# Kernel tuning notes

Measured on AMD Instinct MI355X. Metric: run time of the kernel, lower is better.

The kernel has to match this reference:

```python
import jax, jax.numpy as jnp
import numpy as np
import math

B, Q, K, D = 16, 2048, 2048, 128


def setup_inputs() -> dict:
    key = jax.random.key(0)
    k1, k2, k3, k4 = jax.random.split(key, 4)
    return {
        "queries": jax.random.normal(k1, (B, Q, D), dtype=jnp.float32),
        "keys": jax.random.normal(k2, (B, K, D), dtype=jnp.float32),
        "values": jax.random.normal(k3, (B, K, D), dtype=jnp.float32),
        "valid_lens": jax.random.randint(k4, (B,), 1, K + 1, dtype=jnp.int32),
    }


def reference(queries, keys, values, valid_lens):
    d = queries.shape[2]
    # scores: [B, Q, K]
    scores = jnp.einsum("bqd,bkd->bqk", queries, keys) / math.sqrt(d)
    # mask: arange(K) < valid_lens[b], broadcast over query dim -> [B, 1, K]
    mask = jnp.arange(scores.shape[-1])[None, None, :] < valid_lens[:, None, None]
    scores = jnp.where(mask, scores, jnp.float32(-1000000.0))
    weights = jax.nn.softmax(scores, axis=-1)
    return jnp.einsum("bqk,bkd->bqd", weights, values)
```

## Files before the change

### kernel.cpp

```cpp
#include <hip/hip_runtime.h>

typedef unsigned short u16;
typedef __bf16 bf16x8 __attribute__((ext_vector_type(8)));
typedef float f32x4 __attribute__((ext_vector_type(4)));

union B8 { uint4 u; bf16x8 v; };
union U8 { u16 s[8]; uint4 u; };

#define NQ 2048
#define NK 2048
#define ND 128

template<int C>
__device__ __forceinline__ float dppf(float x) {
  int v = __builtin_bit_cast(int, x);
  int r = __builtin_amdgcn_update_dpp(v, v, C, 0xF, 0xF, true);
  return __builtin_bit_cast(float, r);
}
__device__ __forceinline__ float rowmax16(float x) {
  x = fmaxf(x, dppf<0xB1>(x));
  x = fmaxf(x, dppf<0x4E>(x));
  x = fmaxf(x, dppf<0x141>(x));
  x = fmaxf(x, dppf<0x140>(x));
  return x;
}
__device__ __forceinline__ float rowsum16(float x) {
  x += dppf<0xB1>(x);
  x += dppf<0x4E>(x);
  x += dppf<0x141>(x);
  x += dppf<0x140>(x);
  return x;
}

__device__ __forceinline__ bf16x8 cvt8(float4 a, float4 b) {
  bf16x8 r;
  r[0] = (__bf16)a.x; r[1] = (__bf16)a.y; r[2] = (__bf16)a.z; r[3] = (__bf16)a.w;
  r[4] = (__bf16)b.x; r[5] = (__bf16)b.y; r[6] = (__bf16)b.z; r[7] = (__bf16)b.w;
  return r;
}

__device__ __forceinline__ void async16(const u16* g, u16* l) {
  __builtin_amdgcn_global_load_lds(
      (const __attribute__((address_space(1))) unsigned int*)g,
      (__attribute__((address_space(3))) unsigned int*)l, 16, 0, 0);
}

__global__ __launch_bounds__(256)
void prepack(const float* __restrict__ kg, const float* __restrict__ vg,
             u16* __restrict__ wk, u16* __restrict__ wvp)
{
  __shared__ __align__(16) u16 sVp[8192];
  const int bt  = blockIdx.x;
  const int tid = threadIdx.x;
  const int srow = tid >> 2, scq = tid & 3;
  const size_t rowoff = (size_t)((bt >> 5) * NK + (bt & 31) * 64 + srow) * ND + scq * 32;

  u16* kimg = wk + (size_t)bt * 8192;
  {
    const float* src = kg + rowoff;
    #pragma unroll
    for (int c = 0; c < 4; ++c) {
      B8 tt; tt.v = cvt8(*(const float4*)(src + c * 8), *(const float4*)(src + c * 8 + 4));
      *(uint4*)(&kimg[srow * 128 + (((scq * 4 + c) ^ (srow & 15)) << 3)]) = tt.u;
    }
  }
  {
    const float* src = vg + rowoff;
    #pragma unroll
    for (int c = 0; c < 4; ++c) {
      B8 x; x.v = cvt8(*(const float4*)(src + c * 8), *(const float4*)(src + c * 8 + 4));
      U8 tt; tt.u = x.u;
      #pragma unroll
      for (int j = 0; j < 8; ++j) {
        int d = scq * 32 + c * 8 + j;
        sVp[d * 64 + (((srow >> 3) ^ j) << 3) + (srow & 7)] = tt.s[j];
      }
    }
  }
  __syncthreads();
  u16* vimg = wvp + (size_t)bt * 8192;
  const uint4* s4 = (const uint4*)sVp;
  uint4* d4 = (uint4*)vimg;
  #pragma unroll
  for (int k = 0; k < 4; ++k) d4[tid + 256 * k] = s4[tid + 256 * k];
}

__global__ __launch_bounds__(1024)
void flash_fwd(const float* __restrict__ qg, const int* __restrict__ vlg,
               float* __restrict__ og,
               const u16* __restrict__ wk, const u16* __restrict__ wvp)
{
  __shared__ __align__(16) u16 smem[81920];
  u16* const sKb = smem;
  u16* const sVb = smem + 32768;
  u16* const sPb = smem + 65536;
  float* const fb = (float*)smem;

  const int tid  = threadIdx.x;
  const int lane = tid & 63;
  const int wv   = tid >> 6;
  const int qw   = wv & 7;
  const int grp  = wv >> 3;
  const int n    = lane & 15;
  const int quad = lane >> 4;

  const int bi = blockIdx.x;
  const int b  = ((bi & 7) << 1) | ((bi >> 3) & 1);
  const int qt = bi >> 4;

  const int vl = vlg[b];
  const int nt = (vl + 63) >> 6;

  const int qrow0 = qt * 128 + qw * 16;

  bf16x8 qf[4];
  #pragma unroll
  for (int c = 0; c < 4; ++c) {
    const float* qp = qg + (size_t)(b * NQ + qrow0 + n) * ND + c * 32 + quad * 8;
    qf[c] = cvt8(*(const float4*)qp, *(const float4*)(qp + 4));
  }

  f32x4 O[8];
  float mst[4], lst[4];
  #pragma unroll
  for (int f = 0; f < 8; ++f) O[f] = (f32x4){0.f, 0.f, 0.f, 0.f};
  #pragma unroll
  for (int r = 0; r < 4; ++r) { mst[r] = -__builtin_inff(); lst[r] = 0.f; }

  #define STAGE(t, buf)                                                        \
    do {                                                                       \
      const size_t io_ = (size_t)(b * 32 + (t)) * 8192 + qw * 1024;            \
      const u16* gk_ = wk  + io_ + lane * 8;                                   \
      const u16* gv_ = wvp + io_ + lane * 8;                                   \
      u16* lk_ = sKb + (grp * 2 + (buf)) * 8192 + qw * 1024;                   \
      u16* lv_ = sVb + (grp * 2 + (buf)) * 8192 + qw * 1024;                   \
      async16(gk_,       lk_ + lane * 8);                                      \
      async16(gk_ + 512, lk_ + 512 + lane * 8);                                \
      async16(gv_,       lv_ + lane * 8);                                      \
      async16(gv_ + 512, lv_ + 512 + lane * 8);                                \
    } while (0)

  u16* const Pw = sPb + wv * 1024;

  constexpr float CEXP = 0.08838834764831845f * 1.44269504088896340f;

  if (grp < nt) STAGE(grp, 0);

  const int NS = (nt + 1) >> 1;
  for (int i = 0; i < NS; ++i) {
    __syncthreads();
    const int t  = 2 * i + grp;
    const int tn = t + 2;
    if (tn < nt) STAGE(tn, (i + 1) & 1);

    if (t < nt) {
      const u16* Kg = sKb + (grp * 2 + (i & 1)) * 8192;
      const u16* Vg = sVb + (grp * 2 + (i & 1)) * 8192;

      f32x4 S[4];
      #pragma unroll
      for (int jn = 0; jn < 4; ++jn) S[jn] = (f32x4){0.f, 0.f, 0.f, 0.f};
      #pragma unroll
      for (int c = 0; c < 4; ++c)
        #pragma unroll
        for (int jn = 0; jn < 4; ++jn) {
          B8 bb;
          bb.u = *(const uint4*)(&Kg[(jn * 16 + n) * 128 + (((c * 4 + quad) ^ n) << 3)]);
          S[jn] = __builtin_amdgcn_mfma_f32_16x16x32_bf16(qf[c], bb.v, S[jn], 0, 0, 0);
        }

      if (t * 64 + 64 > vl) {
        #pragma unroll
        for (int jn = 0; jn < 4; ++jn) {
          const bool msk = (t * 64 + jn * 16 + n) >= vl;
          #pragma unroll
          for (int r = 0; r < 4; ++r)
            S[jn][r] = msk ? -1e30f : S[jn][r];
        }
      }

      float al[4];
      #pragma unroll
      for (int r = 0; r < 4; ++r) {
        float mx = fmaxf(fmaxf(S[0][r], S[1][r]), fmaxf(S[2][r], S[3][r]));
        mx = rowmax16(mx);
        float mnew = fmaxf(mst[r], mx);
        float a = __builtin_exp2f((mst[r] - mnew) * CEXP);
        mst[r] = mnew;
        float ssum = 0.f;
        #pragma unroll
        for (int jn = 0; jn < 4; ++jn) {
          float p = __builtin_exp2f((S[jn][r] - mnew) * CEXP);
          S[jn][r] = p;
          ssum += p;
        }
        ssum = rowsum16(ssum);
        lst[r] = lst[r] * a + ssum;
        al[r] = a;
      }
      #pragma unroll
      for (int f = 0; f < 8; ++f) {
        O[f][0] *= al[0]; O[f][1] *= al[1]; O[f][2] *= al[2]; O[f][3] *= al[3];
      }

      #pragma unroll
      for (int jn = 0; jn < 4; ++jn)
        #pragma unroll
        for (int r = 0; r < 4; ++r) {
          int row = quad * 4 + r;
          __bf16 h = (__bf16)S[jn][r];
          Pw[row * 64 + (((jn * 2 + (n >> 3)) ^ (row & 7)) << 3) + (n & 7)]
              = __builtin_bit_cast(u16, h);
        }

      #pragma unroll
      for (int kc = 0; kc < 2; ++kc) {
        B8 ta;
        ta.u = *(const uint4*)(&Pw[n * 64 + (((kc * 4 + quad) ^ (n & 7)) << 3)]);
        bf16x8 af = ta.v;
        #pragma unroll
        for (int f = 0; f < 8; ++f) {
          int d = f * 16 + n;
          B8 bb;
          bb.u = *(const uint4*)(&Vg[d * 64 + (((kc * 4 + quad) ^ (n & 7)) << 3)]);
          O[f] = __builtin_amdgcn_mfma_f32_16x16x32_bf16(af, bb.v, O[f], 0, 0, 0);
        }
      }
    }
  }

  __syncthreads();
  if (grp == 1) {
    float* po = fb + qw * 2048;
    #pragma unroll
    for (int f = 0; f < 8; ++f)
      #pragma unroll
      for (int r = 0; r < 4; ++r)
        po[(quad * 4 + r) * 128 + f * 16 + n] = O[f][r];
    if (n == 0) {
      float* ps = fb + 16384 + qw * 32;
      #pragma unroll
      for (int r = 0; r < 4; ++r) {
        ps[(quad * 4 + r) * 2]     = mst[r];
        ps[(quad * 4 + r) * 2 + 1] = lst[r];
      }
    }
  }
  __syncthreads();
  if (grp == 0) {
    const float* ps = fb + 16384 + qw * 32;
    #pragma unroll
    for (int r = 0; r < 4; ++r) {
      const int row = quad * 4 + r;
      const float m1 = ps[row * 2], l1 = ps[row * 2 + 1];
      const float m  = fmaxf(mst[r], m1);
      const float a0 = __builtin_exp2f((mst[r] - m) * CEXP);
      const float a1 = __builtin_exp2f((m1 - m) * CEXP);
      const float rl = 1.0f / (lst[r] * a0 + l1 * a1);
      float* op = og + (size_t)(b * NQ + qrow0 + row) * ND + n;
      #pragma unroll
      for (int f = 0; f < 8; ++f)
        op[f * 16] = (O[f][r] * a0 + fb[qw * 2048 + row * 128 + f * 16 + n] * a1) * rl;
    }
  }
}

__global__ __launch_bounds__(1024)
void flash_fwd_fb(const float* __restrict__ qg, const float* __restrict__ kg,
                  const float* __restrict__ vg, const int* __restrict__ vlg,
                  float* __restrict__ og)
{
  __shared__ __align__(16) u16 sK[2][64 * 128];
  __shared__ __align__(16) u16 sV[2][64 * 128];
  __shared__ __align__(16) u16 sP[16][16 * 64];

  const int tid  = threadIdx.x;
  const int lane = tid & 63;
  const int wv   = tid >> 6;
  const int qw   = wv & 7;
  const int grp  = wv >> 3;
  const int n    = lane & 15;
  const int quad = lane >> 4;

  const int bi = blockIdx.x;
  const int b  = ((bi & 7) << 1) | ((bi >> 3) & 1);
  const int qt = bi >> 4;

  const int vl = vlg[b];
  const int nt = (vl + 63) >> 6;
  const int qrow0 = qt * 128 + qw * 16;

  bf16x8 qf[4];
  #pragma unroll
  for (int c = 0; c < 4; ++c) {
    const float* qp = qg + (size_t)(b * NQ + qrow0 + n) * ND + c * 32 + quad * 8;
    qf[c] = cvt8(*(const float4*)qp, *(const float4*)(qp + 4));
  }

  f32x4 O[8];
  float mst[4], lst[4];
  #pragma unroll
  for (int f = 0; f < 8; ++f) O[f] = (f32x4){0.f, 0.f, 0.f, 0.f};
  #pragma unroll
  for (int r = 0; r < 4; ++r) { mst[r] = -__builtin_inff(); lst[r] = 0.f; }

  const float* kb = kg + (size_t)(b * NK) * ND;
  const float* vb = vg + (size_t)(b * NK) * ND;
  const int stid = tid & 511;
  const int srow = stid >> 3, sc8 = stid & 7;
  bf16x8 kreg[2], vreg[2];

  auto kload = [&](int t) {
    const float* src = kb + (size_t)(t * 64 + srow) * ND + sc8 * 16;
    #pragma unroll
    for (int c = 0; c < 2; ++c)
      kreg[c] = cvt8(*(const float4*)(src + c * 8), *(const float4*)(src + c * 8 + 4));
  };
  auto kstore = [&]() {
    #pragma unroll
    for (int c = 0; c < 2; ++c) {
      B8 tt; tt.v = kreg[c];
      *(uint4*)(&sK[grp][srow * 128 + (((sc8 * 2 + c) ^ (srow & 15)) << 3)]) = tt.u;
    }
  };
  auto vload = [&](int t) {
    const float* src = vb + (size_t)(t * 64 + srow) * ND + sc8 * 16;
    #pragma unroll
    for (int c = 0; c < 2; ++c)
      vreg[c] = cvt8(*(const float4*)(src + c * 8), *(const float4*)(src + c * 8 + 4));
  };
  auto vstore = [&]() {
    #pragma unroll
    for (int c = 0; c < 2; ++c) {
      B8 x; x.v = vreg[c];
      U8 tt; tt.u = x.u;
      #pragma unroll
      for (int j = 0; j < 8; ++j) {
        int d = sc8 * 16 + c * 8 + j;
        sV[grp][d * 64 + (((srow >> 3) ^ j) << 3) + (srow & 7)] = tt.s[j];
      }
    }
  };

  if (grp < nt) { kload(grp); vload(grp); kstore(); vstore(); }

  constexpr float CEXP = 0.08838834764831845f * 1.44269504088896340f;
  u16* Pw = sP[wv];
  const u16* Kg = sK[grp];
  const u16* Vg = sV[grp];

  const int NS = (nt + 1) >> 1;
  for (int i = 0; i < NS; ++i) {
    __syncthreads();
    const int t  = 2 * i + grp;
    const int tn = t + 2;
    if (tn < nt) { kload(tn); vload(tn); }

    if (t < nt) {
      f32x4 S[4];
      #pragma unroll
      for (int jn = 0; jn < 4; ++jn) S[jn] = (f32x4){0.f, 0.f, 0.f, 0.f};
      #pragma unroll
      for (int c = 0; c < 4; ++c)
        #pragma unroll
        for (int jn = 0; jn < 4; ++jn) {
          B8 bb;
          bb.u = *(const uint4*)(&Kg[(jn * 16 + n) * 128 + (((c * 4 + quad) ^ n) << 3)]);
          S[jn] = __builtin_amdgcn_mfma_f32_16x16x32_bf16(qf[c], bb.v, S[jn], 0, 0, 0);
        }
      if (t * 64 + 64 > vl) {
        #pragma unroll
        for (int jn = 0; jn < 4; ++jn) {
          const bool msk = (t * 64 + jn * 16 + n) >= vl;
          #pragma unroll
          for (int r = 0; r < 4; ++r)
            S[jn][r] = msk ? -1e30f : S[jn][r];
        }
      }
      float al[4];
      #pragma unroll
      for (int r = 0; r < 4; ++r) {
        float mx = fmaxf(fmaxf(S[0][r], S[1][r]), fmaxf(S[2][r], S[3][r]));
        mx = rowmax16(mx);
        float mnew = fmaxf(mst[r], mx);
        float a = __builtin_exp2f((mst[r] - mnew) * CEXP);
        mst[r] = mnew;
        float ssum = 0.f;
        #pragma unroll
        for (int jn = 0; jn < 4; ++jn) {
          float p = __builtin_exp2f((S[jn][r] - mnew) * CEXP);
          S[jn][r] = p;
          ssum += p;
        }
        ssum = rowsum16(ssum);
        lst[r] = lst[r] * a + ssum;
        al[r] = a;
      }
      #pragma unroll
      for (int f = 0; f < 8; ++f) {
        O[f][0] *= al[0]; O[f][1] *= al[1]; O[f][2] *= al[2]; O[f][3] *= al[3];
      }
      #pragma unroll
      for (int jn = 0; jn < 4; ++jn)
        #pragma unroll
        for (int r = 0; r < 4; ++r) {
          int row = quad * 4 + r;
          __bf16 h = (__bf16)S[jn][r];
          Pw[row * 64 + (((jn * 2 + (n >> 3)) ^ (row & 7)) << 3) + (n & 7)]
              = __builtin_bit_cast(u16, h);
        }
      #pragma unroll
      for (int kc = 0; kc < 2; ++kc) {
        B8 ta;
        ta.u = *(const uint4*)(&Pw[n * 64 + (((kc * 4 + quad) ^ (n & 7)) << 3)]);
        bf16x8 af = ta.v;
        #pragma unroll
        for (int f = 0; f < 8; ++f) {
          int d = f * 16 + n;
          B8 bb;
          bb.u = *(const uint4*)(&Vg[d * 64 + (((kc * 4 + quad) ^ (n & 7)) << 3)]);
          O[f] = __builtin_amdgcn_mfma_f32_16x16x32_bf16(af, bb.v, O[f], 0, 0, 0);
        }
      }
    }
    __syncthreads();
    if (tn < nt) { kstore(); vstore(); }
  }

  if (grp == 1) {
    float* ob = ((qw < 4) ? (float*)sK : (float*)sV) + (qw & 3) * 2048 + lane * 32;
    #pragma unroll
    for (int f = 0; f < 8; ++f)
      #pragma unroll
      for (int r = 0; r < 4; ++r)
        ob[f * 4 + r] = O[f][r];
    float* sb = (float*)sP + qw * 512 + lane * 8;
    #pragma unroll
    for (int r = 0; r < 4; ++r) { sb[r] = mst[r]; sb[4 + r] = lst[r]; }
  }
  __syncthreads();
  if (grp == 0) {
    const float* ob = ((qw < 4) ? (const float*)sK : (const float*)sV) + (qw & 3) * 2048 + lane * 32;
    const float* sb = (const float*)sP + qw * 512 + lane * 8;
    #pragma unroll
    for (int r = 0; r < 4; ++r) {
      const float m1 = sb[r], l1 = sb[4 + r];
      const float m  = fmaxf(mst[r], m1);
      const float a0 = __builtin_exp2f((mst[r] - m) * CEXP);
      const float a1 = __builtin_exp2f((m1 - m) * CEXP);
      const float rl = 1.0f / (lst[r] * a0 + l1 * a1);
      const int qrow = qrow0 + quad * 4 + r;
      float* op = og + (size_t)(b * NQ + qrow) * ND + n;
      #pragma unroll
      for (int f = 0; f < 8; ++f)
        op[f * 16] = (O[f][r] * a0 + ob[f * 4 + r] * a1) * rl;
    }
  }
}

extern "C" void kernel_launch(void* const* d_in, const int* in_sizes, int n_in,
                              void* d_out, int out_size, void* d_ws, size_t ws_size,
                              hipStream_t stream) {
  const float* q  = (const float*)d_in[0];
  const float* k  = (const float*)d_in[1];
  const float* v  = (const float*)d_in[2];
  const int*  vl  = (const int*)d_in[3];
  float* out = (float*)d_out;

  const size_t need = (size_t)16 * 1024 * 1024;
  if (ws_size >= need) {
    u16* wk  = (u16*)d_ws;
    u16* wvv = wk + 4194304;
    hipLaunchKernelGGL(prepack, dim3(512), dim3(256), 0, stream, k, v, wk, wvv);
    hipLaunchKernelGGL(flash_fwd, dim3(256), dim3(1024), 0, stream, q, vl, out, wk, wvv);
  } else {
    hipLaunchKernelGGL(flash_fwd_fb, dim3(256), dim3(1024), 0, stream, q, k, v, vl, out);
  }
}
```

Before: 165.7 us.

## Give each wave two 16-row query blocks and coalesce output stores via LDS

Halves the block to 512 threads (8 waves) and has each wave process 32 query rows as two 16-row MFMA blocks. Each K and V fragment read from LDS then feeds two MFMAs, which halves LDS read traffic per FLOP. The final combine is staged in shared memory and written out as coalesced float4 stores. The cost is roughly double the accumulator and score registers per wave, which adds spill or occupancy risk, and fewer waves are left to hide latency.

```diff
diff --git a/kernel.cpp b/kernel.cpp
--- a/kernel.cpp
+++ b/kernel.cpp
@@ -85,7 +85,7 @@
   for (int k = 0; k < 4; ++k) d4[tid + 256 * k] = s4[tid + 256 * k];
 }
 
-__global__ __launch_bounds__(1024)
+__global__ __launch_bounds__(512, 2)
 void flash_fwd(const float* __restrict__ qg, const int* __restrict__ vlg,
                float* __restrict__ og,
                const u16* __restrict__ wk, const u16* __restrict__ wvp)
@@ -99,8 +99,8 @@
   const int tid  = threadIdx.x;
   const int lane = tid & 63;
   const int wv   = tid >> 6;
-  const int qw   = wv & 7;
-  const int grp  = wv >> 3;
+  const int qw   = wv & 3;
+  const int grp  = wv >> 2;
   const int n    = lane & 15;
   const int quad = lane >> 4;
 
@@ -111,36 +111,42 @@
   const int vl = vlg[b];
   const int nt = (vl + 63) >> 6;
 
-  const int qrow0 = qt * 128 + qw * 16;
-
-  bf16x8 qf[4];
+  const int qrow0 = qt * 128 + qw * 32;
+
+  bf16x8 qf[2][4];
   #pragma unroll
-  for (int c = 0; c < 4; ++c) {
-    const float* qp = qg + (size_t)(b * NQ + qrow0 + n) * ND + c * 32 + quad * 8;
-    qf[c] = cvt8(*(const float4*)qp, *(const float4*)(qp + 4));
-  }
-
-  f32x4 O[8];
-  float mst[4], lst[4];
+  for (int mb = 0; mb < 2; ++mb)
+    #pragma unroll
+    for (int c = 0; c < 4; ++c) {
+      const float* qp = qg + (size_t)(b * NQ + qrow0 + mb * 16 + n) * ND + c * 32 + quad * 8;
+      qf[mb][c] = cvt8(*(const float4*)qp, *(const float4*)(qp + 4));
+    }
+
+  f32x4 O[2][8];
+  float mst[2][4], lst[2][4];
   #pragma unroll
-  for (int f = 0; f < 8; ++f) O[f] = (f32x4){0.f, 0.f, 0.f, 0.f};
-  #pragma unroll
-  for (int r = 0; r < 4; ++r) { mst[r] = -__builtin_inff(); lst[r] = 0.f; }
+  for (int mb = 0; mb < 2; ++mb) {
+    #pragma unroll
+    for (int f = 0; f < 8; ++f) O[mb][f] = (f32x4){0.f, 0.f, 0.f, 0.f};
+    #pragma unroll
+    for (int r = 0; r < 4; ++r) { mst[mb][r] = -__builtin_inff(); lst[mb][r] = 0.f; }
+  }
 
   #define STAGE(t, buf)                                                        \
     do {                                                                       \
-      const size_t io_ = (size_t)(b * 32 + (t)) * 8192 + qw * 1024;            \
+      const size_t io_ = (size_t)(b * 32 + (t)) * 8192 + qw * 2048;            \
       const u16* gk_ = wk  + io_ + lane * 8;                                   \
       const u16* gv_ = wvp + io_ + lane * 8;                                   \
-      u16* lk_ = sKb + (grp * 2 + (buf)) * 8192 + qw * 1024;                   \
-      u16* lv_ = sVb + (grp * 2 + (buf)) * 8192 + qw * 1024;                   \
-      async16(gk_,       lk_ + lane * 8);                                      \
-      async16(gk_ + 512, lk_ + 512 + lane * 8);                                \
-      async16(gv_,       lv_ + lane * 8);                                      \
-      async16(gv_ + 512, lv_ + 512 + lane * 8);                                \
+      u16* lk_ = sKb + (grp * 2 + (buf)) * 8192 + qw * 2048;                   \
+      u16* lv_ = sVb + (grp * 2 + (buf)) * 8192 + qw * 2048;                   \
+      _Pragma("unroll")                                                        \
+      for (int j_ = 0; j_ < 4; ++j_) {                                         \
+        async16(gk_ + j_ * 512, lk_ + j_ * 512 + lane * 8);                    \
+        async16(gv_ + j_ * 512, lv_ + j_ * 512 + lane * 8);                    \
+      }                                                                        \
     } while (0)
 
-  u16* const Pw = sPb + wv * 1024;
+  u16* const Pw = sPb + wv * 2048;
 
   constexpr float CEXP = 0.08838834764831845f * 1.44269504088896340f;
 
@@ -157,16 +163,19 @@
       const u16* Kg = sKb + (grp * 2 + (i & 1)) * 8192;
       const u16* Vg = sVb + (grp * 2 + (i & 1)) * 8192;
 
-      f32x4 S[4];
-      #pragma unroll
-      for (int jn = 0; jn < 4; ++jn) S[jn] = (f32x4){0.f, 0.f, 0.f, 0.f};
+      f32x4 S[2][4];
+      #pragma unroll
+      for (int mb = 0; mb < 2; ++mb)
+        #pragma unroll
+        for (int jn = 0; jn < 4; ++jn) S[mb][jn] = (f32x4){0.f, 0.f, 0.f, 0.f};
       #pragma unroll
       for (int c = 0; c < 4; ++c)
         #pragma unroll
         for (int jn = 0; jn < 4; ++jn) {
           B8 bb;
           bb.u = *(const uint4*)(&Kg[(jn * 16 + n) * 128 + (((c * 4 + quad) ^ n) << 3)]);
-          S[jn] = __builtin_amdgcn_mfma_f32_16x16x32_bf16(qf[c], bb.v, S[jn], 0, 0, 0);
+          S[0][jn] = __builtin_amdgcn_mfma_f32_16x16x32_bf16(qf[0][c], bb.v, S[0][jn], 0, 0, 0);
+          S[1][jn] = __builtin_amdgcn_mfma_f32_16x16x32_bf16(qf[1][c], bb.v, S[1][jn], 0, 0, 0);
         }
 
       if (t * 64 + 64 > vl) {
@@ -174,94 +183,122 @@
         for (int jn = 0; jn < 4; ++jn) {
           const bool msk = (t * 64 + jn * 16 + n) >= vl;
           #pragma unroll
-          for (int r = 0; r < 4; ++r)
-            S[jn][r] = msk ? -1e30f : S[jn][r];
-        }
-      }
-
-      float al[4];
-      #pragma unroll
-      for (int r = 0; r < 4; ++r) {
-        float mx = fmaxf(fmaxf(S[0][r], S[1][r]), fmaxf(S[2][r], S[3][r]));
-        mx = rowmax16(mx);
-        float mnew = fmaxf(mst[r], mx);
-        float a = __builtin_exp2f((mst[r] - mnew) * CEXP);
-        mst[r] = mnew;
-        float ssum = 0.f;
-        #pragma unroll
-        for (int jn = 0; jn < 4; ++jn) {
-          float p = __builtin_exp2f((S[jn][r] - mnew) * CEXP);
-          S[jn][r] = p;
-          ssum += p;
-        }
-        ssum = rowsum16(ssum);
-        lst[r] = lst[r] * a + ssum;
-        al[r] = a;
-      }
-      #pragma unroll
-      for (int f = 0; f < 8; ++f) {
-        O[f][0] *= al[0]; O[f][1] *= al[1]; O[f][2] *= al[2]; O[f][3] *= al[3];
-      }
-
-      #pragma unroll
-      for (int jn = 0; jn < 4; ++jn)
+          for (int r = 0; r < 4; ++r) {
+            S[0][jn][r] = msk ? -1e30f : S[0][jn][r];
+            S[1][jn][r] = msk ? -1e30f : S[1][jn][r];
+          }
+        }
+      }
+
+      float al[2][4];
+      #pragma unroll
+      for (int mb = 0; mb < 2; ++mb)
         #pragma unroll
         for (int r = 0; r < 4; ++r) {
-          int row = quad * 4 + r;
-          __bf16 h = (__bf16)S[jn][r];
-          Pw[row * 64 + (((jn * 2 + (n >> 3)) ^ (row & 7)) << 3) + (n & 7)]
-              = __builtin_bit_cast(u16, h);
-        }
+          float mx = fmaxf(fmaxf(S[mb][0][r], S[mb][1][r]), fmaxf(S[mb][2][r], S[mb][3][r]));
+          mx = rowmax16(mx);
+          float mnew = fmaxf(mst[mb][r], mx);
+          float a = __builtin_exp2f((mst[mb][r] - mnew) * CEXP);
+          mst[mb][r] = mnew;
+          float ssum = 0.f;
+          #pragma unroll
+          for (int jn = 0; jn < 4; ++jn) {
+            float p = __builtin_exp2f((S[mb][jn][r] - mnew) * CEXP);
+            S[mb][jn][r] = p;
+            ssum += p;
+          }
+          ssum = rowsum16(ssum);
+          lst[mb][r] = lst[mb][r] * a + ssum;
+          al[mb][r] = a;
+        }
+      #pragma unroll
+      for (int mb = 0; mb < 2; ++mb)
+        #pragma unroll
+        for (int f = 0; f < 8; ++f) {
+          O[mb][f][0] *= al[mb][0]; O[mb][f][1] *= al[mb][1];
+          O[mb][f][2] *= al[mb][2]; O[mb][f][3] *= al[mb][3];
+        }
+
+      #pragma unroll
+      for (int mb = 0; mb < 2; ++mb)
+        #pragma unroll
+        for (int jn = 0; jn < 4; ++jn)
+          #pragma unroll
+          for (int r = 0; r < 4; ++r) {
+            int row = mb * 16 + quad * 4 + r;
+            __bf16 h = (__bf16)S[mb][jn][r];
+            Pw[row * 64 + (((jn * 2 + (n >> 3)) ^ (row & 7)) << 3) + (n & 7)]
+                = __builtin_bit_cast(u16, h);
+          }
 
       #pragma unroll
       for (int kc = 0; kc < 2; ++kc) {
-        B8 ta;
-        ta.u = *(const uint4*)(&Pw[n * 64 + (((kc * 4 + quad) ^ (n & 7)) << 3)]);
-        bf16x8 af = ta.v;
+        bf16x8 af[2];
+        #pragma unroll
+        for (int mb = 0; mb < 2; ++mb) {
+          B8 ta;
+          ta.u = *(const uint4*)(&Pw[(mb * 16 + n) * 64 + (((kc * 4 + quad) ^ (n & 7)) << 3)]);
+          af[mb] = ta.v;
+        }
         #pragma unroll
         for (int f = 0; f < 8; ++f) {
           int d = f * 16 + n;
           B8 bb;
           bb.u = *(const uint4*)(&Vg[d * 64 + (((kc * 4 + quad) ^ (n & 7)) << 3)]);
-          O[f] = __builtin_amdgcn_mfma_f32_16x16x32_bf16(af, bb.v, O[f], 0, 0, 0);
-        }
-      }
-    }
-  }
+          O[0][f] = __builtin_amdgcn_mfma_f32_16x16x32_bf16(af[0], bb.v, O[0][f], 0, 0, 0);
+          O[1][f] = __builtin_amdgcn_mfma_f32_16x16x32_bf16(af[1], bb.v, O[1][f], 0, 0, 0);
+        }
+      }
+    }
+  }
+  #undef STAGE
 
   __syncthreads();
+  float* const ps = fb + 16384;
   if (grp == 1) {
-    float* po = fb + qw * 2048;
-    #pragma unroll
-    for (int f = 0; f < 8; ++f)
-      #pragma unroll
-      for (int r = 0; r < 4; ++r)
-        po[(quad * 4 + r) * 128 + f * 16 + n] = O[f][r];
-    if (n == 0) {
-      float* ps = fb + 16384 + qw * 32;
-      #pragma unroll
-      for (int r = 0; r < 4; ++r) {
-        ps[(quad * 4 + r) * 2]     = mst[r];
-        ps[(quad * 4 + r) * 2 + 1] = lst[r];
+    #pragma unroll
+    for (int mb = 0; mb < 2; ++mb) {
+      #pragma unroll
+      for (int f = 0; f < 8; ++f)
+        #pragma unroll
+        for (int r = 0; r < 4; ++r)
+          fb[(qw * 32 + mb * 16 + quad * 4 + r) * 128 + f * 16 + n] = O[mb][f][r];
+      if (n == 0) {
+        #pragma unroll
+        for (int r = 0; r < 4; ++r) {
+          const int row = qw * 32 + mb * 16 + quad * 4 + r;
+          ps[row * 2]     = mst[mb][r];
+          ps[row * 2 + 1] = lst[mb][r];
+        }
       }
     }
   }
   __syncthreads();
   if (grp == 0) {
-    const float* ps = fb + 16384 + qw * 32;
-    #pragma unroll
-    for (int r = 0; r < 4; ++r) {
-      const int row = quad * 4 + r;
-      const float m1 = ps[row * 2], l1 = ps[row * 2 + 1];
-      const float m  = fmaxf(mst[r], m1);
-      const float a0 = __builtin_exp2f((mst[r] - m) * CEXP);
-      const float a1 = __builtin_exp2f((m1 - m) * CEXP);
-      const float rl = 1.0f / (lst[r] * a0 + l1 * a1);
-      float* op = og + (size_t)(b * NQ + qrow0 + row) * ND + n;
-      #pragma unroll
-      for (int f = 0; f < 8; ++f)
-        op[f * 16] = (O[f][r] * a0 + fb[qw * 2048 + row * 128 + f * 16 + n] * a1) * rl;
-    }
+    #pragma unroll
+    for (int mb = 0; mb < 2; ++mb)
+      #pragma unroll
+      for (int r = 0; r < 4; ++r) {
+        const int row = qw * 32 + mb * 16 + quad * 4 + r;
+        const float m1 = ps[row * 2], l1 = ps[row * 2 + 1];
+        const float m  = fmaxf(mst[mb][r], m1);
+        const float a0 = __builtin_exp2f((mst[mb][r] - m) * CEXP);
+        const float a1 = __builtin_exp2f((m1 - m) * CEXP);
+        const float rl = 1.0f / (lst[mb][r] * a0 + l1 * a1);
+        #pragma unroll
+        for (int f = 0; f < 8; ++f) {
+          const int idx = row * 128 + f * 16 + n;
+          fb[idx] = (O[mb][f][r] * a0 + fb[idx] * a1) * rl;
+        }
+      }
+  }
+  __syncthreads();
+  {
+    const float4* s4 = (const float4*)fb;
+    float4* d4 = (float4*)(og + (size_t)(b * NQ + qt * 128) * ND);
+    #pragma unroll
+    for (int k = 0; k < 8; ++k)
+      d4[tid + 512 * k] = s4[tid + 512 * k];
   }
 }
 
@@ -472,7 +509,7 @@
     u16* wk  = (u16*)d_ws;
     u16* wvv = wk + 4194304;
     hipLaunchKernelGGL(prepack, dim3(512), dim3(256), 0, stream, k, v, wk, wvv);
-    hipLaunchKernelGGL(flash_fwd, dim3(256), dim3(1024), 0, stream, q, vl, out, wk, wvv);
+    hipLaunchKernelGGL(flash_fwd, dim3(256), dim3(512), 0, stream, q, vl, out, wk, wvv);
   } else {
     hipLaunchKernelGGL(flash_fwd_fb, dim3(256), dim3(1024), 0, stream, q, k, v, vl, out);
   }
```

Result: no change. 162.6 us (-1.9%).

## Split key range into chunks across blocks with last-block merge of partials

Applied to the files above, without the earlier changes.

Replaces the single 1024-thread kernel, which split keys between two wave groups inside one block, with a 512-thread kernel launched over 1024 blocks. Each block handles one 512-key chunk of one query tile. Blocks write partial O, max and sum to workspace, and an atomic counter picks the last-finishing block to rescale and merge the partials. This is meant to even out the load imbalance from variable valid lengths and raise occupancy. It adds global traffic for the partials, a memset and a larger 82 MB workspace requirement; if the workspace is smaller, the slow fallback kernel runs. It also adds s_setprio hints around the MFMA sections.

```diff
diff --git a/kernel.cpp b/kernel.cpp
--- a/kernel.cpp
+++ b/kernel.cpp
@@ -44,6 +44,8 @@
       (const __attribute__((address_space(1))) unsigned int*)g,
       (__attribute__((address_space(3))) unsigned int*)l, 16, 0, 0);
 }
+
+constexpr float CEXP = 0.08838834764831845f * 1.44269504088896340f;
 
 __global__ __launch_bounds__(256)
 void prepack(const float* __restrict__ kg, const float* __restrict__ vg,
@@ -85,16 +87,240 @@
   for (int k = 0; k < 4; ++k) d4[tid + 256 * k] = s4[tid + 256 * k];
 }
 
+__global__ __launch_bounds__(512, 2)
+void flash_chunk3(const float* __restrict__ qg, const int* __restrict__ vlg,
+                  const u16* __restrict__ wk, const u16* __restrict__ wvp,
+                  float* __restrict__ pO, float* __restrict__ pML,
+                  int* __restrict__ done, float* __restrict__ og)
+{
+  __shared__ __align__(16) u16 sK[2][8192];
+  __shared__ __align__(16) u16 sV[2][8192];
+  __shared__ __align__(16) u16 sP[8][1024];
+
+  const int tid  = threadIdx.x;
+  const int lane = tid & 63;
+  const int wv   = tid >> 6;
+  const int n    = lane & 15;
+  const int quad = lane >> 4;
+
+  const int bi   = blockIdx.x;
+  const int b    = ((bi & 7) << 1) | ((bi >> 3) & 1);
+  const int qt   = (bi >> 4) & 15;
+  const int ck   = bi >> 8;
+
+  const int vl = vlg[b];
+  const int nt = (vl + 63) >> 6;
+  const int t0 = ck * 8;
+  if (t0 >= nt) return;
+  const int t1 = (t0 + 8 < nt) ? (t0 + 8) : nt;
+  const int nc = (nt + 7) >> 3;
+
+  const int qrow0 = qt * 128 + wv * 16;
+
+  bf16x8 qf[4];
+  #pragma unroll
+  for (int c = 0; c < 4; ++c) {
+    const float* qp = qg + (size_t)(b * NQ + qrow0 + n) * ND + c * 32 + quad * 8;
+    qf[c] = cvt8(*(const float4*)qp, *(const float4*)(qp + 4));
+  }
+
+  f32x4 O[8];
+  float mst[4], lst[4];
+  #pragma unroll
+  for (int f = 0; f < 8; ++f) O[f] = (f32x4){0.f, 0.f, 0.f, 0.f};
+  #pragma unroll
+  for (int r = 0; r < 4; ++r) { mst[r] = -__builtin_inff(); lst[r] = 0.f; }
+
+  #define STAGE(t, buf)                                                        \
+    do {                                                                       \
+      const size_t io_ = (size_t)(b * 32 + (t)) * 8192 + wv * 1024;            \
+      const u16* gk_ = wk  + io_ + lane * 8;                                   \
+      const u16* gv_ = wvp + io_ + lane * 8;                                   \
+      u16* lk_ = sK[(buf)] + wv * 1024 + lane * 8;                             \
+      u16* lv_ = sV[(buf)] + wv * 1024 + lane * 8;                             \
+      async16(gk_,       lk_);                                                 \
+      async16(gk_ + 512, lk_ + 512);                                           \
+      async16(gv_,       lv_);                                                 \
+      async16(gv_ + 512, lv_ + 512);                                           \
+    } while (0)
+
+  u16* const Pw = sP[wv];
+
+  STAGE(t0, 0);
+
+  for (int t = t0; t < t1; ++t) {
+    __syncthreads();
+    if (t + 1 < t1) STAGE(t + 1, (t - t0 + 1) & 1);
+
+    const u16* Kg = sK[(t - t0) & 1];
+    const u16* Vg = sV[(t - t0) & 1];
+
+    f32x4 S[4];
+    #pragma unroll
+    for (int jn = 0; jn < 4; ++jn) S[jn] = (f32x4){0.f, 0.f, 0.f, 0.f};
+    __builtin_amdgcn_s_setprio(1);
+    #pragma unroll
+    for (int c = 0; c < 4; ++c)
+      #pragma unroll
+      for (int jn = 0; jn < 4; ++jn) {
+        B8 bb;
+        bb.u = *(const uint4*)(&Kg[(jn * 16 + n) * 128 + (((c * 4 + quad) ^ n) << 3)]);
+        S[jn] = __builtin_amdgcn_mfma_f32_16x16x32_bf16(qf[c], bb.v, S[jn], 0, 0, 0);
+      }
+    __builtin_amdgcn_s_setprio(0);
+
+    if (t * 64 + 64 > vl) {
+      #pragma unroll
+      for (int jn = 0; jn < 4; ++jn) {
+        const bool msk = (t * 64 + jn * 16 + n) >= vl;
+        #pragma unroll
+        for (int r = 0; r < 4; ++r)
+          S[jn][r] = msk ? -1e30f : S[jn][r];
+      }
+    }
+
+    float al[4];
+    #pragma unroll
+    for (int r = 0; r < 4; ++r) {
+      float mx = fmaxf(fmaxf(S[0][r], S[1][r]), fmaxf(S[2][r], S[3][r]));
+      mx = rowmax16(mx);
+      float mnew = fmaxf(mst[r], mx);
+      float a = __builtin_exp2f((mst[r] - mnew) * CEXP);
+      mst[r] = mnew;
+      float ssum = 0.f;
+      #pragma unroll
+      for (int jn = 0; jn < 4; ++jn) {
+        float p = __builtin_exp2f((S[jn][r] - mnew) * CEXP);
+        S[jn][r] = p;
+        ssum += p;
+      }
+      ssum = rowsum16(ssum);
+      lst[r] = lst[r] * a + ssum;
+      al[r] = a;
+    }
+    #pragma unroll
+    for (int f = 0; f < 8; ++f) {
+      O[f][0] *= al[0]; O[f][1] *= al[1]; O[f][2] *= al[2]; O[f][3] *= al[3];
+    }
+
+    #pragma unroll
+    for (int jn = 0; jn < 4; ++jn)
+      #pragma unroll
+      for (int r = 0; r < 4; ++r) {
+        int row = quad * 4 + r;
+        __bf16 h = (__bf16)S[jn][r];
+        Pw[row * 64 + (((jn * 2 + (n >> 3)) ^ (row & 7)) << 3) + (n & 7)]
+            = __builtin_bit_cast(u16, h);
+      }
+
+    __builtin_amdgcn_s_setprio(1);
+    #pragma unroll
+    for (int kc = 0; kc < 2; ++kc) {
+      B8 ta;
+      ta.u = *(const uint4*)(&Pw[n * 64 + (((kc * 4 + quad) ^ (n & 7)) << 3)]);
+      bf16x8 af = ta.v;
+      #pragma unroll
+      for (int f = 0; f < 8; ++f) {
+        int d = f * 16 + n;
+        B8 bb;
+        bb.u = *(const uint4*)(&Vg[d * 64 + (((kc * 4 + quad) ^ (n & 7)) << 3)]);
+        O[f] = __builtin_amdgcn_mfma_f32_16x16x32_bf16(af, bb.v, O[f], 0, 0, 0);
+      }
+    }
+    __builtin_amdgcn_s_setprio(0);
+  }
+  #undef STAGE
+
+  if (nc == 1) {
+    #pragma unroll
+    for (int r = 0; r < 4; ++r) {
+      const float rl = 1.0f / lst[r];
+      const int qrow = qrow0 + quad * 4 + r;
+      float* op = og + (size_t)(b * NQ + qrow) * ND + n;
+      #pragma unroll
+      for (int f = 0; f < 8; ++f)
+        op[f * 16] = O[f][r] * rl;
+    }
+    return;
+  }
+
+  const size_t ti = (size_t)((b * 16 + qt) * 4 + ck);
+  float* po = pO + ti * 16384;
+  #pragma unroll
+  for (int f = 0; f < 8; ++f)
+    #pragma unroll
+    for (int r = 0; r < 4; ++r)
+      po[(wv * 16 + quad * 4 + r) * 128 + f * 16 + n] = O[f][r];
+  if (n == 0) {
+    float* ps = pML + ti * 256;
+    #pragma unroll
+    for (int r = 0; r < 4; ++r) {
+      const int row = wv * 16 + quad * 4 + r;
+      ps[row * 2]     = mst[r];
+      ps[row * 2 + 1] = lst[r];
+    }
+  }
+
+  float* const wts   = (float*)sP;
+  int*   const winfl = (int*)sP + 512;
+
+  __threadfence();
+  __syncthreads();
+  if (tid == 0) {
+    const int old = atomicAdd(&done[b * 16 + qt], 1);
+    *winfl = (old + 1 == nc);
+  }
+  __syncthreads();
+  if (!*winfl) return;
+  __threadfence();
+
+  const size_t ti0 = (size_t)(b * 16 + qt) * 4;
+  if (tid < 128) {
+    const int row = tid;
+    float m[4], l[4];
+    float mx = -__builtin_inff();
+    for (int c = 0; c < nc; ++c) {
+      m[c] = pML[(ti0 + c) * 256 + row * 2];
+      l[c] = pML[(ti0 + c) * 256 + row * 2 + 1];
+      mx = fmaxf(mx, m[c]);
+    }
+    float L = 0.f;
+    float a[4];
+    for (int c = 0; c < nc; ++c) {
+      a[c] = __builtin_exp2f((m[c] - mx) * CEXP);
+      L += l[c] * a[c];
+    }
+    const float inv = 1.0f / L;
+    #pragma unroll
+    for (int c = 0; c < 4; ++c)
+      wts[row * 4 + c] = (c < nc) ? a[c] * inv : 0.f;
+  }
+  __syncthreads();
+
+  const float4* p4 = (const float4*)(pO + ti0 * 16384);
+  float4* o4 = (float4*)(og + (size_t)(b * NQ + qt * 128) * ND);
+  #pragma unroll
+  for (int it = 0; it < 8; ++it) {
+    const int gi  = it * 512 + tid;
+    const int row = gi >> 5;
+    float4 acc = {0.f, 0.f, 0.f, 0.f};
+    for (int c = 0; c < nc; ++c) {
+      const float4 x = p4[c * 4096 + gi];
+      const float s = wts[row * 4 + c];
+      acc.x += x.x * s; acc.y += x.y * s; acc.z += x.z * s; acc.w += x.w * s;
+    }
+    o4[gi] = acc;
+  }
+}
+
 __global__ __launch_bounds__(1024)
-void flash_fwd(const float* __restrict__ qg, const int* __restrict__ vlg,
-               float* __restrict__ og,
-               const u16* __restrict__ wk, const u16* __restrict__ wvp)
+void flash_fwd_fb(const float* __restrict__ qg, const float* __restrict__ kg,
+                  const float* __restrict__ vg, const int* __restrict__ vlg,
+                  float* __restrict__ og)
 {
-  __shared__ __align__(16) u16 smem[81920];
-  u16* const sKb = smem;
-  u16* const sVb = smem + 32768;
-  u16* const sPb = smem + 65536;
-  float* const fb = (float*)smem;
+  __shared__ __align__(16) u16 sK[2][64 * 128];
+  __shared__ __align__(16) u16 sV[2][64 * 128];
+  __shared__ __align__(16) u16 sP[16][16 * 64];
 
   const int tid  = threadIdx.x;
   const int lane = tid & 63;
@@ -110,7 +336,6 @@
 
   const int vl = vlg[b];
   const int nt = (vl + 63) >> 6;
-
   const int qrow0 = qt * 128 + qw * 16;
 
   bf16x8 qf[4];
@@ -127,36 +352,58 @@
   #pragma unroll
   for (int r = 0; r < 4; ++r) { mst[r] = -__builtin_inff(); lst[r] = 0.f; }
 
-  #define STAGE(t, buf)                                                        \
-    do {                                                                       \
-      const size_t io_ = (size_t)(b * 32 + (t)) * 8192 + qw * 1024;            \
-      const u16* gk_ = wk  + io_ + lane * 8;                                   \
-      const u16* gv_ = wvp + io_ + lane * 8;                                   \
-      u16* lk_ = sKb + (grp * 2 + (buf)) * 8192 + qw * 1024;                   \
-      u16* lv_ = sVb + (grp * 2 + (buf)) * 8192 + qw * 1024;                   \
-      async16(gk_,       lk_ + lane * 8);                                      \
-      async16(gk_ + 512, lk_ + 512 + lane * 8);                                \
-      async16(gv_,       lv_ + lane * 8);                                      \
-      async16(gv_ + 512, lv_ + 512 + lane * 8);                                \
-    } while (0)
-
-  u16* const Pw = sPb + wv * 1024;
-
-  constexpr float CEXP = 0.08838834764831845f * 1.44269504088896340f;
-
-  if (grp < nt) STAGE(grp, 0);
+  const float* kb = kg + (size_t)(b * NK) * ND;
+  const float* vb = vg + (size_t)(b * NK) * ND;
+  const int stid = tid & 511;
+  const int srow = stid >> 3, sc8 = stid & 7;
+  bf16x8 kreg[2], vreg[2];
+
+  auto kload = [&](int t) {
+    const float* src = kb + (size_t)(t * 64 + srow) * ND + sc8 * 16;
+    #pragma unroll
+    for (int c = 0; c < 2; ++c)
+      kreg[c] = cvt8(*(const float4*)(src + c * 8), *(const float4*)(src + c * 8 + 4));
+  };
+  auto kstore = [&]() {
+    #pragma unroll
+    for (int c = 0; c < 2; ++c) {
+      B8 tt; tt.v = kreg[c];
+      *(uint4*)(&sK[grp][srow * 128 + (((sc8 * 2 + c) ^ (srow & 15)) << 3)]) = tt.u;
+    }
+  };
+  auto vload = [&](int t) {
+    const float* src = vb + (size_t)(t * 64 + srow) * ND + sc8 * 16;
+    #pragma unroll
+    for (int c = 0; c < 2; ++c)
+      vreg[c] = cvt8(*(const float4*)(src + c * 8), *(const float4*)(src + c * 8 + 4));
+  };
+  auto vstore = [&]() {
+    #pragma unroll
+    for (int c = 0; c < 2; ++c) {
+      B8 x; x.v = vreg[c];
+      U8 tt; tt.u = x.u;
+      #pragma unroll
+      for (int j = 0; j < 8; ++j) {
+        int d = sc8 * 16 + c * 8 + j;
+        sV[grp][d * 64 + (((srow >> 3) ^ j) << 3) + (srow & 7)] = tt.s[j];
+      }
+    }
+  };
+
+  if (grp < nt) { kload(grp); vload(grp); kstore(); vstore(); }
+
+  u16* Pw = sP[wv];
+  const u16* Kg = sK[grp];
+  const u16* Vg = sV[grp];
 
   const int NS = (nt + 1) >> 1;
   for (int i = 0; i < NS; ++i) {
     __syncthreads();
     const int t  = 2 * i + grp;
     const int tn = t + 2;
-    if (tn < nt) STAGE(tn, (i + 1) & 1);
+    if (tn < nt) { kload(tn); vload(tn); }
 
     if (t < nt) {
-      const u16* Kg = sKb + (grp * 2 + (i & 1)) * 8192;
-      const u16* Vg = sVb + (grp * 2 + (i & 1)) * 8192;
-
       f32x4 S[4];
       #pragma unroll
       for (int jn = 0; jn < 4; ++jn) S[jn] = (f32x4){0.f, 0.f, 0.f, 0.f};
@@ -168,7 +415,6 @@
           bb.u = *(const uint4*)(&Kg[(jn * 16 + n) * 128 + (((c * 4 + quad) ^ n) << 3)]);
           S[jn] = __builtin_amdgcn_mfma_f32_16x16x32_bf16(qf[c], bb.v, S[jn], 0, 0, 0);
         }
-
       if (t * 64 + 64 > vl) {
         #pragma unroll
         for (int jn = 0; jn < 4; ++jn) {
@@ -178,7 +424,6 @@
             S[jn][r] = msk ? -1e30f : S[jn][r];
         }
       }
-
       float al[4];
       #pragma unroll
       for (int r = 0; r < 4; ++r) {
@@ -202,7 +447,6 @@
       for (int f = 0; f < 8; ++f) {
         O[f][0] *= al[0]; O[f][1] *= al[1]; O[f][2] *= al[2]; O[f][3] *= al[3];
       }
-
       #pragma unroll
       for (int jn = 0; jn < 4; ++jn)
         #pragma unroll
@@ -212,7 +456,6 @@
           Pw[row * 64 + (((jn * 2 + (n >> 3)) ^ (row & 7)) << 3) + (n & 7)]
               = __builtin_bit_cast(u16, h);
         }
-
       #pragma unroll
       for (int kc = 0; kc < 2; ++kc) {
         B8 ta;
@@ -227,202 +470,6 @@
         }
       }
     }
-  }
-
-  __syncthreads();
-  if (grp == 1) {
-    float* po = fb + qw * 2048;
-    #pragma unroll
-    for (int f = 0; f < 8; ++f)
-      #pragma unroll
-      for (int r = 0; r < 4; ++r)
-        po[(quad * 4 + r) * 128 + f * 16 + n] = O[f][r];
-    if (n == 0) {
-      float* ps = fb + 16384 + qw * 32;
-      #pragma unroll
-      for (int r = 0; r < 4; ++r) {
-        ps[(quad * 4 + r) * 2]     = mst[r];
-        ps[(quad * 4 + r) * 2 + 1] = lst[r];
-      }
-    }
-  }
-  __syncthreads();
-  if (grp == 0) {
-    const float* ps = fb + 16384 + qw * 32;
-    #pragma unroll
-    for (int r = 0; r < 4; ++r) {
-      const int row = quad * 4 + r;
-      const float m1 = ps[row * 2], l1 = ps[row * 2 + 1];
-      const float m  = fmaxf(mst[r], m1);
-      const float a0 = __builtin_exp2f((mst[r] - m) * CEXP);
-      const float a1 = __builtin_exp2f((m1 - m) * CEXP);
-      const float rl = 1.0f / (lst[r] * a0 + l1 * a1);
-      float* op = og + (size_t)(b * NQ + qrow0 + row) * ND + n;
-      #pragma unroll
-      for (int f = 0; f < 8; ++f)
-        op[f * 16] = (O[f][r] * a0 + fb[qw * 2048 + row * 128 + f * 16 + n] * a1) * rl;
-    }
-  }
-}
-
-__global__ __launch_bounds__(1024)
-void flash_fwd_fb(const float* __restrict__ qg, const float* __restrict__ kg,
-                  const float* __restrict__ vg, const int* __restrict__ vlg,
-                  float* __restrict__ og)
-{
-  __shared__ __align__(16) u16 sK[2][64 * 128];
-  __shared__ __align__(16) u16 sV[2][64 * 128];
-  __shared__ __align__(16) u16 sP[16][16 * 64];
-
-  const int tid  = threadIdx.x;
-  const int lane = tid & 63;
-  const int wv   = tid >> 6;
-  const int qw   = wv & 7;
-  const int grp  = wv >> 3;
-  const int n    = lane & 15;
-  const int quad = lane >> 4;
-
-  const int bi = blockIdx.x;
-  const int b  = ((bi & 7) << 1) | ((bi >> 3) & 1);
-  const int qt = bi >> 4;
-
-  const int vl = vlg[b];
-  const int nt = (vl + 63) >> 6;
-  const int qrow0 = qt * 128 + qw * 16;
-
-  bf16x8 qf[4];
-  #pragma unroll
-  for (int c = 0; c < 4; ++c) {
-    const float* qp = qg + (size_t)(b * NQ + qrow0 + n) * ND + c * 32 + quad * 8;
-    qf[c] = cvt8(*(const float4*)qp, *(const float4*)(qp + 4));
-  }
-
-  f32x4 O[8];
-  float mst[4], lst[4];
-  #pragma unroll
-  for (int f = 0; f < 8; ++f) O[f] = (f32x4){0.f, 0.f, 0.f, 0.f};
-  #pragma unroll
-  for (int r = 0; r < 4; ++r) { mst[r] = -__builtin_inff(); lst[r] = 0.f; }
-
-  const float* kb = kg + (size_t)(b * NK) * ND;
-  const float* vb = vg + (size_t)(b * NK) * ND;
-  const int stid = tid & 511;
-  const int srow = stid >> 3, sc8 = stid & 7;
-  bf16x8 kreg[2], vreg[2];
-
-  auto kload = [&](int t) {
-    const float* src = kb + (size_t)(t * 64 + srow) * ND + sc8 * 16;
-    #pragma unroll
-    for (int c = 0; c < 2; ++c)
-      kreg[c] = cvt8(*(const float4*)(src + c * 8), *(const float4*)(src + c * 8 + 4));
-  };
-  auto kstore = [&]() {
-    #pragma unroll
-    for (int c = 0; c < 2; ++c) {
-      B8 tt; tt.v = kreg[c];
-      *(uint4*)(&sK[grp][srow * 128 + (((sc8 * 2 + c) ^ (srow & 15)) << 3)]) = tt.u;
-    }
-  };
-  auto vload = [&](int t) {
-    const float* src = vb + (size_t)(t * 64 + srow) * ND + sc8 * 16;
-    #pragma unroll
-    for (int c = 0; c < 2; ++c)
-      vreg[c] = cvt8(*(const float4*)(src + c * 8), *(const float4*)(src + c * 8 + 4));
-  };
-  auto vstore = [&]() {
-    #pragma unroll
-    for (int c = 0; c < 2; ++c) {
-      B8 x; x.v = vreg[c];
-      U8 tt; tt.u = x.u;
-      #pragma unroll
-      for (int j = 0; j < 8; ++j) {
-        int d = sc8 * 16 + c * 8 + j;
-        sV[grp][d * 64 + (((srow >> 3) ^ j) << 3) + (srow & 7)] = tt.s[j];
-      }
-    }
-  };
-
-  if (grp < nt) { kload(grp); vload(grp); kstore(); vstore(); }
-
-  constexpr float CEXP = 0.08838834764831845f * 1.44269504088896340f;
-  u16* Pw = sP[wv];
-  const u16* Kg = sK[grp];
-  const u16* Vg = sV[grp];
-
-  const int NS = (nt + 1) >> 1;
-  for (int i = 0; i < NS; ++i) {
-    __syncthreads();
-    const int t  = 2 * i + grp;
-    const int tn = t + 2;
-    if (tn < nt) { kload(tn); vload(tn); }
-
-    if (t < nt) {
-      f32x4 S[4];
-      #pragma unroll
-      for (int jn = 0; jn < 4; ++jn) S[jn] = (f32x4){0.f, 0.f, 0.f, 0.f};
-      #pragma unroll
-      for (int c = 0; c < 4; ++c)
-        #pragma unroll
-        for (int jn = 0; jn < 4; ++jn) {
-          B8 bb;
-          bb.u = *(const uint4*)(&Kg[(jn * 16 + n) * 128 + (((c * 4 + quad) ^ n) << 3)]);
-          S[jn] = __builtin_amdgcn_mfma_f32_16x16x32_bf16(qf[c], bb.v, S[jn], 0, 0, 0);
-        }
-      if (t * 64 + 64 > vl) {
-        #pragma unroll
-        for (int jn = 0; jn < 4; ++jn) {
-          const bool msk = (t * 64 + jn * 16 + n) >= vl;
-          #pragma unroll
-          for (int r = 0; r < 4; ++r)
-            S[jn][r] = msk ? -1e30f : S[jn][r];
-        }
-      }
-      float al[4];
-      #pragma unroll
-      for (int r = 0; r < 4; ++r) {
-        float mx = fmaxf(fmaxf(S[0][r], S[1][r]), fmaxf(S[2][r], S[3][r]));
-        mx = rowmax16(mx);
-        float mnew = fmaxf(mst[r], mx);
-        float a = __builtin_exp2f((mst[r] - mnew) * CEXP);
-        mst[r] = mnew;
-        float ssum = 0.f;
-        #pragma unroll
-        for (int jn = 0; jn < 4; ++jn) {
-          float p = __builtin_exp2f((S[jn][r] - mnew) * CEXP);
-          S[jn][r] = p;
-          ssum += p;
-        }
-        ssum = rowsum16(ssum);
-        lst[r] = lst[r] * a + ssum;
-        al[r] = a;
-      }
-      #pragma unroll
-      for (int f = 0; f < 8; ++f) {
-        O[f][0] *= al[0]; O[f][1] *= al[1]; O[f][2] *= al[2]; O[f][3] *= al[3];
-      }
-      #pragma unroll
-      for (int jn = 0; jn < 4; ++jn)
-        #pragma unroll
-        for (int r = 0; r < 4; ++r) {
-          int row = quad * 4 + r;
-          __bf16 h = (__bf16)S[jn][r];
-          Pw[row * 64 + (((jn * 2 + (n >> 3)) ^ (row & 7)) << 3) + (n & 7)]
-              = __builtin_bit_cast(u16, h);
-        }
-      #pragma unroll
-      for (int kc = 0; kc < 2; ++kc) {
-        B8 ta;
-        ta.u = *(const uint4*)(&Pw[n * 64 + (((kc * 4 + quad) ^ (n & 7)) << 3)]);
-        bf16x8 af = ta.v;
-        #pragma unroll
-        for (int f = 0; f < 8; ++f) {
-          int d = f * 16 + n;
-          B8 bb;
-          bb.u = *(const uint4*)(&Vg[d * 64 + (((kc * 4 + quad) ^ (n & 7)) << 3)]);
-          O[f] = __builtin_amdgcn_mfma_f32_16x16x32_bf16(af, bb.v, O[f], 0, 0, 0);
-        }
-      }
-    }
     __syncthreads();
     if (tn < nt) { kstore(); vstore(); }
   }
@@ -467,12 +514,18 @@
   const int*  vl  = (const int*)d_in[3];
   float* out = (float*)d_out;
 
-  const size_t need = (size_t)16 * 1024 * 1024;
-  if (ws_size >= need) {
-    u16* wk  = (u16*)d_ws;
-    u16* wvv = wk + 4194304;
+  const size_t need_split = (size_t)82 * 1024 * 1024;
+
+  if (ws_size >= need_split) {
+    u16*   wk  = (u16*)d_ws;
+    u16*   wvv = wk + 4194304;
+    float* pO  = (float*)((char*)d_ws + (size_t)16 * 1024 * 1024);
+    float* pML = (float*)((char*)d_ws + (size_t)80 * 1024 * 1024);
+    int*   dn  = (int*)  ((char*)d_ws + (size_t)81 * 1024 * 1024);
+    hipMemsetAsync(dn, 0, 1024, stream);
     hipLaunchKernelGGL(prepack, dim3(512), dim3(256), 0, stream, k, v, wk, wvv);
-    hipLaunchKernelGGL(flash_fwd, dim3(256), dim3(1024), 0, stream, q, vl, out, wk, wvv);
+    hipLaunchKernelGGL(flash_chunk3, dim3(1024), dim3(512), 0, stream,
+                       q, vl, wk, wvv, pO, pML, dn, out);
   } else {
     hipLaunchKernelGGL(flash_fwd_fb, dim3(256), dim3(1024), 0, stream, q, k, v, vl, out);
   }
```

Result: slower. 423.5 us (+155.6%).
